# Kernel optimization log

Hardware: AMD Instinct MI355X
Metric: run time of the kernel (lower is better)

The kernel has to match this reference:

```python
import jax, jax.numpy as jnp
import numpy as np

CH = 128
MID = CH // 4  # 32
B, H, W = 16, 128, 128


def _phi(x):
    # elu(x) + 1 (alpha=1)
    return jax.nn.elu(x) + 1.0


def setup_inputs() -> dict:
    key = jax.random.key(0)
    ks = jax.random.split(key, 6)
    x = jax.random.normal(ks[0], (B, CH, H, W), dtype=jnp.float32)
    Wq = jax.random.normal(ks[1], (MID, CH), dtype=jnp.float32) * 0.05
    Wk = jax.random.normal(ks[2], (MID, CH), dtype=jnp.float32) * 0.05
    Wv = jax.random.normal(ks[3], (MID, CH), dtype=jnp.float32) * 0.05
    Wout = jax.random.normal(ks[4], (CH, MID), dtype=jnp.float32) * 0.05
    gamma = jnp.ones((CH,), dtype=jnp.float32)
    beta = jnp.zeros((CH,), dtype=jnp.float32)
    return {"x": x, "Wq": Wq, "Wk": Wk, "Wv": Wv, "Wout": Wout,
            "gamma": gamma, "beta": beta}


def reference(x, Wq, Wk, Wv, Wout, gamma, beta):
    b, c, h, w = x.shape
    n = h * w
    xf = x.reshape(b, c, n)                      # [B, C, N]
    # 1x1 convs == channel matmuls
    Q = _phi(jnp.einsum('mc,bcn->bmn', Wq, xf))  # [B, M, N]
    K = _phi(jnp.einsum('mc,bcn->bmn', Wk, xf))  # [B, M, N]
    V = jnp.einsum('mc,bcn->bmn', Wv, xf)        # [B, M, N]
    # KV-first linear attention
    KV = jnp.einsum('bmn,bvn->bmv', K, V)        # [B, M, M]
    out = jnp.einsum('bmv,bvn->bmn', KV, Q) / (n + 1e-6)  # [B, M, N]
    Ks = jnp.sum(K, axis=-1, keepdims=True)      # [B, M, 1]
    denom = jnp.sum(Q * Ks, axis=1, keepdims=True) + 1e-6  # [B, 1, N]
    out = out / denom
    # output 1x1 conv
    y = jnp.einsum('cm,bmn->bcn', Wout, out).reshape(b, c, h, w)
    # BatchNorm2d (training-mode forward: batch statistics, biased var, eps=1e-5)
    mean = jnp.mean(y, axis=(0, 2, 3), keepdims=True)
    var = jnp.var(y, axis=(0, 2, 3), keepdims=True)
    y = (y - mean) * jax.lax.rsqrt(var + 1e-5)
    y = y * gamma[None, :, None, None] + beta[None, :, None, None]
    return y
```

## Files before the change

### kernel.cpp

```cpp
#include <hip/hip_runtime.h>

#define BB 16
#define CC 128
#define MM 32
#define NN 16384

#define WS_KV     0
#define WS_KS     16384
#define WS_SQ     16896
#define WS_QQ     17408
#define WS_YSUM   33792
#define WS_YSQ    33920
#define WS_ACCEND 34048
#define WS_W2     34304

typedef __bf16 bf16x8 __attribute__((ext_vector_type(8)));
typedef __bf16 bf16x4 __attribute__((ext_vector_type(4)));
typedef float  f32x16 __attribute__((ext_vector_type(16)));

union B8 { bf16x8 v8; bf16x4 v4[2]; };

__device__ __forceinline__ float phi_f(float z) {
    return z > 0.f ? z + 1.f : __expf(z);
}

__global__ void zero_kernel(float* ws) {
    const int i = blockIdx.x * 256 + threadIdx.x;
    if (i < (WS_ACCEND / 4)) {
        float4 z; z.x = 0.f; z.y = 0.f; z.z = 0.f; z.w = 0.f;
        ((float4*)ws)[i] = z;
    }
}

__global__ __launch_bounds__(256) void projmfma_kernel(
    const float* __restrict__ x,
    const float* __restrict__ Wq, const float* __restrict__ Wk,
    const float* __restrict__ Wv,
    float* ws, float* __restrict__ qout)
{
    __shared__ __align__(16) char smem[55296];
    __bf16* Xh  = (__bf16*)smem;
    __bf16* Xl  = (__bf16*)(smem + 17408);
    __bf16* ktH = (__bf16*)(smem + 34816);
    __bf16* ktL = (__bf16*)(smem + 39936);
    __bf16* vtH = (__bf16*)(smem + 45056);
    __bf16* vtL = (__bf16*)(smem + 50176);

    const int b = blockIdx.y;
    const int t = threadIdx.x;
    const int w = t >> 6;
    const int l = t & 63;
    const int g = l >> 5;
    const int ln31 = l & 31;

    bf16x8 wh[8], wl[8];
    if (w < 3) {
        const float* Wm = (w == 0) ? Wq : (w == 1) ? Wk : Wv;
        const float* wr = Wm + ln31 * CC;
        #pragma unroll
        for (int kt = 0; kt < 8; ++kt) {
            const int k0 = 16 * kt + 8 * g;
            #pragma unroll
            for (int j = 0; j < 8; ++j) {
                const float f = wr[k0 + j];
                const __bf16 h = (__bf16)f;
                wh[kt][j] = h;
                wl[kt][j] = (__bf16)(f - (float)h);
            }
        }
    }

    f32x16 kvA, ksA;
    bf16x8 ones;
    #pragma unroll
    for (int i = 0; i < 16; ++i) { kvA[i] = 0.f; ksA[i] = 0.f; }
    #pragma unroll
    for (int j = 0; j < 8; ++j) ones[j] = (__bf16)1.0f;

    const int px = t & 31;
    const int cb = t >> 5;

    const float* xbase = x + (size_t)b * CC * NN + (blockIdx.x << 9) + px;

    float xbuf[16];
    #pragma unroll
    for (int j = 0; j < 16; ++j)
        xbuf[j] = xbase[(size_t)(cb * 16 + j) * NN];
    {
        __bf16 hbuf[16], lbuf[16];
        #pragma unroll
        for (int j = 0; j < 16; ++j) {
            const float f = xbuf[j];
            const __bf16 h = (__bf16)f;
            hbuf[j] = h;
            lbuf[j] = (__bf16)(f - (float)h);
        }
        *(bf16x8*)&Xh[px * 136 + cb * 16]     = *(bf16x8*)&hbuf[0];
        *(bf16x8*)&Xh[px * 136 + cb * 16 + 8] = *(bf16x8*)&hbuf[8];
        *(bf16x8*)&Xl[px * 136 + cb * 16]     = *(bf16x8*)&lbuf[0];
        *(bf16x8*)&Xl[px * 136 + cb * 16 + 8] = *(bf16x8*)&lbuf[8];
    }
    __syncthreads();

    for (int tile = 0; tile < 16; ++tile) {
        const int cur = tile & 1;
        const int n0 = (blockIdx.x << 9) + (tile << 5);

        if (tile < 15) {
            const float* xp = xbase + ((tile + 1) << 5);
            #pragma unroll
            for (int j = 0; j < 16; ++j)
                xbuf[j] = xp[(size_t)(cb * 16 + j) * NN];
        }

        f32x16 acc;
        if (w < 3) {
            #pragma unroll
            for (int i = 0; i < 16; ++i) acc[i] = 0.f;
            const __bf16* xh = Xh + cur * 4352 + ln31 * 136;
            const __bf16* xl = Xl + cur * 4352 + ln31 * 136;
            #pragma unroll
            for (int kt = 0; kt < 8; ++kt) {
                const int k0 = 16 * kt + 8 * g;
                const bf16x8 bh = *(const bf16x8*)&xh[k0];
                const bf16x8 bl = *(const bf16x8*)&xl[k0];
                acc = __builtin_amdgcn_mfma_f32_32x32x16_bf16(wh[kt], bh, acc, 0, 0, 0);
                acc = __builtin_amdgcn_mfma_f32_32x32x16_bf16(wh[kt], bl, acc, 0, 0, 0);
                acc = __builtin_amdgcn_mfma_f32_32x32x16_bf16(wl[kt], bh, acc, 0, 0, 0);
            }
        } else if (tile > 0) {
            const int pbuf = (cur ^ 1) * 1280;
            const __bf16* khp = ktH + pbuf + ln31 * 40;
            const __bf16* klp = ktL + pbuf + ln31 * 40;
            const __bf16* vhp = vtH + pbuf + ln31 * 40;
            const __bf16* vlp = vtL + pbuf + ln31 * 40;
            #pragma unroll
            for (int s = 0; s < 2; ++s) {
                const int k0 = s * 16 + g * 8;
                const bf16x8 akh = *(const bf16x8*)&khp[k0];
                const bf16x8 akl = *(const bf16x8*)&klp[k0];
                const bf16x8 bvh = *(const bf16x8*)&vhp[k0];
                const bf16x8 bvl = *(const bf16x8*)&vlp[k0];
                kvA = __builtin_amdgcn_mfma_f32_32x32x16_bf16(akh, bvh, kvA, 0, 0, 0);
                kvA = __builtin_amdgcn_mfma_f32_32x32x16_bf16(akh, bvl, kvA, 0, 0, 0);
                kvA = __builtin_amdgcn_mfma_f32_32x32x16_bf16(akl, bvh, kvA, 0, 0, 0);
                ksA = __builtin_amdgcn_mfma_f32_32x32x16_bf16(akh, ones, ksA, 0, 0, 0);
                ksA = __builtin_amdgcn_mfma_f32_32x32x16_bf16(akl, ones, ksA, 0, 0, 0);
            }
        }

        if (w == 0) {
            float* qp = qout + (size_t)b * CC * NN + n0 + ln31;
            #pragma unroll
            for (int i = 0; i < 16; ++i) {
                const int r = (i & 3) + 8 * (i >> 2) + 4 * g;
                qp[(size_t)r * NN] = phi_f(acc[i]);
            }
        } else if (w == 1) {
            __bf16* kh = ktH + cur * 1280;
            __bf16* kl = ktL + cur * 1280;
            #pragma unroll
            for (int i = 0; i < 16; ++i) {
                const int r = (i & 3) + 8 * (i >> 2) + 4 * g;
                const float f = phi_f(acc[i]);
                const __bf16 h = (__bf16)f;
                kh[r * 40 + ln31] = h;
                kl[r * 40 + ln31] = (__bf16)(f - (float)h);
            }
        } else if (w == 2) {
            __bf16* vh = vtH + cur * 1280;
            __bf16* vl = vtL + cur * 1280;
            #pragma unroll
            for (int i = 0; i < 16; ++i) {
                const int r = (i & 3) + 8 * (i >> 2) + 4 * g;
                const float f = acc[i];
                const __bf16 h = (__bf16)f;
                vh[r * 40 + ln31] = h;
                vl[r * 40 + ln31] = (__bf16)(f - (float)h);
            }
        }

        if (tile < 15) {
            const int nxt = cur ^ 1;
            __bf16 hbuf[16], lbuf[16];
            #pragma unroll
            for (int j = 0; j < 16; ++j) {
                const float f = xbuf[j];
                const __bf16 h = (__bf16)f;
                hbuf[j] = h;
                lbuf[j] = (__bf16)(f - (float)h);
            }
            *(bf16x8*)&Xh[nxt * 4352 + px * 136 + cb * 16]     = *(bf16x8*)&hbuf[0];
            *(bf16x8*)&Xh[nxt * 4352 + px * 136 + cb * 16 + 8] = *(bf16x8*)&hbuf[8];
            *(bf16x8*)&Xl[nxt * 4352 + px * 136 + cb * 16]     = *(bf16x8*)&lbuf[0];
            *(bf16x8*)&Xl[nxt * 4352 + px * 136 + cb * 16 + 8] = *(bf16x8*)&lbuf[8];
        }
        __syncthreads();
    }

    if (w == 3) {
        const int pbuf = 1280;
        const __bf16* khp = ktH + pbuf + ln31 * 40;
        const __bf16* klp = ktL + pbuf + ln31 * 40;
        const __bf16* vhp = vtH + pbuf + ln31 * 40;
        const __bf16* vlp = vtL + pbuf + ln31 * 40;
        #pragma unroll
        for (int s = 0; s < 2; ++s) {
            const int k0 = s * 16 + g * 8;
            const bf16x8 akh = *(const bf16x8*)&khp[k0];
            const bf16x8 akl = *(const bf16x8*)&klp[k0];
            const bf16x8 bvh = *(const bf16x8*)&vhp[k0];
            const bf16x8 bvl = *(const bf16x8*)&vlp[k0];
            kvA = __builtin_amdgcn_mfma_f32_32x32x16_bf16(akh, bvh, kvA, 0, 0, 0);
            kvA = __builtin_amdgcn_mfma_f32_32x32x16_bf16(akh, bvl, kvA, 0, 0, 0);
            kvA = __builtin_amdgcn_mfma_f32_32x32x16_bf16(akl, bvh, kvA, 0, 0, 0);
            ksA = __builtin_amdgcn_mfma_f32_32x32x16_bf16(akh, ones, ksA, 0, 0, 0);
            ksA = __builtin_amdgcn_mfma_f32_32x32x16_bf16(akl, ones, ksA, 0, 0, 0);
        }
        float* kvb = ws + WS_KV + (b << 10);
        #pragma unroll
        for (int i = 0; i < 16; ++i) {
            const int r = (i & 3) + 8 * (i >> 2) + 4 * g;
            atomicAdd(&kvb[r * 32 + ln31], kvA[i]);
        }
        if (ln31 == 0) {
            #pragma unroll
            for (int i = 0; i < 16; ++i) {
                const int r = (i & 3) + 8 * (i >> 2) + 4 * g;
                atomicAdd(&ws[WS_KS + (b << 5) + r], ksA[i]);
            }
        }
    }
}

__global__ __launch_bounds__(256) void qq_kernel(const float* qsrc, float* ws) {
    __shared__ __align__(16) char qsm[33792];
    __bf16* Qh = (__bf16*)qsm;
    __bf16* Ql = (__bf16*)(qsm + 16896);
    float*  red   = (float*)qsm;
    float*  sqred = (float*)(qsm + 17408);

    const int b = blockIdx.y;
    const int t = threadIdx.x;
    const int w = t >> 6;
    const int l = t & 63;
    const int g = l >> 5;
    const int ln31 = l & 31;

    const float* ksb = ws + WS_KS + (b << 5);
    const int n = (blockIdx.x << 8) + t;
    const float* qp = qsrc + (size_t)b * CC * NN + n;

    float qa[32];
    #pragma unroll
    for (int m = 0; m < 32; ++m) qa[m] = qp[(size_t)m * NN];

    float denom = 1e-6f;
    #pragma unroll
    for (int m = 0; m < 32; ++m) denom = fmaf(qa[m], ksb[m], denom);
    const float inv = 1.0f / (16384.0f * denom);
    #pragma unroll
    for (int m = 0; m < 32; ++m) qa[m] *= inv;

    #pragma unroll
    for (int m = 0; m < 32; ++m) {
        const __bf16 h = (__bf16)qa[m];
        Qh[m * 264 + t] = h;
        Ql[m * 264 + t] = (__bf16)(qa[m] - (float)h);
    }
    __syncthreads();

    f32x16 qqA, sqA;
    bf16x8 ones;
    #pragma unroll
    for (int i = 0; i < 16; ++i) { qqA[i] = 0.f; sqA[i] = 0.f; }
    #pragma unroll
    for (int j = 0; j < 8; ++j) ones[j] = (__bf16)1.0f;

    #pragma unroll
    for (int sub = 0; sub < 2; ++sub) {
        #pragma unroll
        for (int s = 0; s < 2; ++s) {
            const int k0 = (w << 6) + (sub << 5) + s * 16 + g * 8;
            const bf16x8 ah = *(const bf16x8*)&Qh[ln31 * 264 + k0];
            const bf16x8 al = *(const bf16x8*)&Ql[ln31 * 264 + k0];
            qqA = __builtin_amdgcn_mfma_f32_32x32x16_bf16(ah, ah, qqA, 0, 0, 0);
            qqA = __builtin_amdgcn_mfma_f32_32x32x16_bf16(ah, al, qqA, 0, 0, 0);
            qqA = __builtin_amdgcn_mfma_f32_32x32x16_bf16(al, ah, qqA, 0, 0, 0);
            sqA = __builtin_amdgcn_mfma_f32_32x32x16_bf16(ah, ones, sqA, 0, 0, 0);
            sqA = __builtin_amdgcn_mfma_f32_32x32x16_bf16(al, ones, sqA, 0, 0, 0);
        }
    }
    __syncthreads();

    #pragma unroll
    for (int i = 0; i < 16; ++i) red[t * 17 + i] = qqA[i];
    if (ln31 == 0) {
        #pragma unroll
        for (int i = 0; i < 16; ++i) {
            const int r = (i & 3) + 8 * (i >> 2) + 4 * g;
            sqred[(w << 5) + r] = sqA[i];
        }
    }
    __syncthreads();
    if (t < 64) {
        float* qqb = ws + WS_QQ + (b << 10);
        #pragma unroll
        for (int i = 0; i < 16; ++i) {
            const int r = (i & 3) + 8 * (i >> 2) + 4 * g;
            const float s = red[t*17+i] + red[(t+64)*17+i] + red[(t+128)*17+i] + red[(t+192)*17+i];
            atomicAdd(&qqb[r * 32 + ln31], s);
        }
    }
    if (t < 32) {
        const float s = sqred[t] + sqred[32 + t] + sqred[64 + t] + sqred[96 + t];
        atomicAdd(&ws[WS_SQ + (b << 5) + t], s);
    }
}

__global__ __launch_bounds__(128) void bnstat_kernel(const float* __restrict__ Wout,
                                                     float* ws) {
    const int b = blockIdx.x;
    const int c = threadIdx.x;
    const float* kvb = ws + WS_KV + (b << 10);
    const float* wo  = Wout + (c << 5);
    float w[32];
    #pragma unroll
    for (int v = 0; v < 32; ++v) w[v] = 0.f;
    for (int m = 0; m < 32; ++m) {
        const float wm = wo[m];
        #pragma unroll
        for (int v = 0; v < 32; ++v) w[v] = fmaf(wm, kvb[(m << 5) + v], w[v]);
    }
    float* w2b = ws + WS_W2 + (b << 12) + (c << 5);
    #pragma unroll
    for (int v = 0; v < 32; ++v) w2b[v] = w[v];

    const float* sq = ws + WS_SQ + (b << 5);
    const float* qq = ws + WS_QQ + (b << 10);
    float mb = 0.f;
    #pragma unroll
    for (int v = 0; v < 32; ++v) mb = fmaf(w[v], sq[v], mb);
    float qf = 0.f;
    for (int u = 0; u < 32; ++u) {
        float tacc = 0.f;
        #pragma unroll
        for (int v = 0; v < 32; ++v) tacc = fmaf(qq[(u << 5) + v], w[v], tacc);
        qf = fmaf(w[u], tacc, qf);
    }
    atomicAdd(&ws[WS_YSUM + c], mb);
    atomicAdd(&ws[WS_YSQ + c], qf);
}

__global__ __launch_bounds__(256) void out_kernel(const float* qsrc, const float* ws,
                                                  const float* __restrict__ gamma,
                                                  const float* __restrict__ beta,
                                                  float* out) {
    __shared__ __align__(16) __bf16 Qh[256 * 36];
    __shared__ __align__(16) __bf16 Ql[256 * 36];
    __shared__ float scs[CC];
    __shared__ float bis[CC];

    const int b = blockIdx.y;
    const int t = threadIdx.x;
    const int w = t >> 6;
    const int l = t & 63;
    const int g = l >> 5;
    const int ln31 = l & 31;

    if (t < CC) {
        const float invBN = 1.0f / 262144.0f;
        const float mean = ws[WS_YSUM + t] * invBN;
        const float var  = ws[WS_YSQ + t] * invBN - mean * mean;
        const float s = gamma[t] * rsqrtf(var + 1e-5f);
        scs[t] = s;
        bis[t] = fmaf(-mean, s, beta[t]);
    }

    const int n = (blockIdx.x << 8) + t;
    const float* ksb = ws + WS_KS + (b << 5);

    const float* qp = qsrc + (size_t)b * CC * NN + n;
    float qa[32];
    #pragma unroll
    for (int m = 0; m < 32; ++m) qa[m] = qp[(size_t)m * NN];

    float d0 = 1e-6f;
    #pragma unroll
    for (int m = 0; m < 32; ++m) d0 = fmaf(qa[m], ksb[m], d0);
    const float inv = 1.0f / (16384.0f * d0);
    #pragma unroll
    for (int m = 0; m < 32; ++m) qa[m] *= inv;

    {
        __bf16 qh[32], ql[32];
        #pragma unroll
        for (int m = 0; m < 32; ++m) {
            const __bf16 h = (__bf16)qa[m];
            qh[m] = h;
            ql[m] = (__bf16)(qa[m] - (float)h);
        }
        #pragma unroll
        for (int i = 0; i < 8; ++i) {
            *(bf16x4*)&Qh[t * 36 + i * 4] = *(bf16x4*)&qh[i * 4];
            *(bf16x4*)&Ql[t * 36 + i * 4] = *(bf16x4*)&ql[i * 4];
        }
    }
    __syncthreads();

    const float* w2b = ws + WS_W2 + (b << 12);
    float* ob = out + (size_t)b * CC * NN + (blockIdx.x << 8);

    #pragma unroll
    for (int cb = 0; cb < 4; ++cb) {
        bf16x8 ah[2], al[2];
        #pragma unroll
        for (int kt = 0; kt < 2; ++kt) {
            const float* wp = w2b + (cb * 32 + ln31) * 32 + kt * 16 + g * 8;
            #pragma unroll
            for (int j = 0; j < 8; ++j) {
                const float f = wp[j];
                const __bf16 h = (__bf16)f;
                ah[kt][j] = h;
                al[kt][j] = (__bf16)(f - (float)h);
            }
        }
        #pragma unroll
        for (int pg = 0; pg < 2; ++pg) {
            const int px0 = (w << 6) + (pg << 5);
            f32x16 acc;
            #pragma unroll
            for (int i = 0; i < 16; ++i) acc[i] = 0.f;
            #pragma unroll
            for (int kt = 0; kt < 2; ++kt) {
                const int k0 = kt * 16 + g * 8;
                const __bf16* qhp = &Qh[(px0 + ln31) * 36 + k0];
                const __bf16* qlp = &Ql[(px0 + ln31) * 36 + k0];
                B8 bh, bl;
                bh.v4[0] = *(const bf16x4*)&qhp[0];
                bh.v4[1] = *(const bf16x4*)&qhp[4];
                bl.v4[0] = *(const bf16x4*)&qlp[0];
                bl.v4[1] = *(const bf16x4*)&qlp[4];
                acc = __builtin_amdgcn_mfma_f32_32x32x16_bf16(ah[kt], bh.v8, acc, 0, 0, 0);
                acc = __builtin_amdgcn_mfma_f32_32x32x16_bf16(ah[kt], bl.v8, acc, 0, 0, 0);
                acc = __builtin_amdgcn_mfma_f32_32x32x16_bf16(al[kt], bh.v8, acc, 0, 0, 0);
            }
            #pragma unroll
            for (int i = 0; i < 16; ++i) {
                const int r = (i & 3) + 8 * (i >> 2) + 4 * g;
                const int c = cb * 32 + r;
                const float v = fmaf(scs[c], acc[i], bis[c]);
                __builtin_nontemporal_store(v, &ob[(size_t)c * NN + px0 + ln31]);
            }
        }
    }
}

extern "C" void kernel_launch(void* const* d_in, const int* in_sizes, int n_in,
                              void* d_out, int out_size, void* d_ws, size_t ws_size,
                              hipStream_t stream) {
    const float* x     = (const float*)d_in[0];
    const float* Wq    = (const float*)d_in[1];
    const float* Wk    = (const float*)d_in[2];
    const float* Wv    = (const float*)d_in[3];
    const float* Wout  = (const float*)d_in[4];
    const float* gamma = (const float*)d_in[5];
    const float* beta  = (const float*)d_in[6];
    float* ws  = (float*)d_ws;
    float* out = (float*)d_out;

    zero_kernel<<<34, 256, 0, stream>>>(ws);
    projmfma_kernel<<<dim3(32, 16), 256, 0, stream>>>(x, Wq, Wk, Wv, ws, out);
    qq_kernel<<<dim3(64, 16), 256, 0, stream>>>(out, ws);
    bnstat_kernel<<<16, 128, 0, stream>>>(Wout, ws);
    out_kernel<<<dim3(64, 16), 256, 0, stream>>>(out, ws, gamma, beta, out);
}
```

Baseline: 114.2 us.

## Double projection block to 512 threads processing two pixel tiles per step

The projection kernel now runs 8 waves per block: two groups of four waves each handle one of two 32-pixel sub-tiles, so each loop step covers 64 pixels in 8 steps instead of 16. The x double-buffer is replaced by a single two-half staging buffer with an extra barrier per step, and the K/V transposed buffers are quadrupled in LDS. The aim is more waves in flight per CU and fewer loop iterations to hide global-load latency. In exchange LDS use grows to about 74KB, which may cap blocks per CU, and each wave group's final KV atomics double.

```diff
diff --git a/kernel.cpp b/kernel.cpp
--- a/kernel.cpp
+++ b/kernel.cpp
@@ -32,19 +32,19 @@
     }
 }
 
-__global__ __launch_bounds__(256) void projmfma_kernel(
+__global__ __launch_bounds__(512) void projmfma_kernel(
     const float* __restrict__ x,
     const float* __restrict__ Wq, const float* __restrict__ Wk,
     const float* __restrict__ Wv,
     float* ws, float* __restrict__ qout)
 {
-    __shared__ __align__(16) char smem[55296];
+    __shared__ __align__(16) char smem[75776];
     __bf16* Xh  = (__bf16*)smem;
     __bf16* Xl  = (__bf16*)(smem + 17408);
     __bf16* ktH = (__bf16*)(smem + 34816);
-    __bf16* ktL = (__bf16*)(smem + 39936);
-    __bf16* vtH = (__bf16*)(smem + 45056);
-    __bf16* vtL = (__bf16*)(smem + 50176);
+    __bf16* ktL = (__bf16*)(smem + 45056);
+    __bf16* vtH = (__bf16*)(smem + 55296);
+    __bf16* vtL = (__bf16*)(smem + 65536);
 
     const int b = blockIdx.y;
     const int t = threadIdx.x;
@@ -52,10 +52,12 @@
     const int l = t & 63;
     const int g = l >> 5;
     const int ln31 = l & 31;
+    const int wsel = w & 3;
+    const int tb = (w >> 2) & 1;
 
     bf16x8 wh[8], wl[8];
-    if (w < 3) {
-        const float* Wm = (w == 0) ? Wq : (w == 1) ? Wk : Wv;
+    if (wsel < 3) {
+        const float* Wm = (wsel == 0) ? Wq : (wsel == 1) ? Wk : Wv;
         const float* wr = Wm + ln31 * CC;
         #pragma unroll
         for (int kt = 0; kt < 8; ++kt) {
@@ -77,48 +79,52 @@
     #pragma unroll
     for (int j = 0; j < 8; ++j) ones[j] = (__bf16)1.0f;
 
-    const int px = t & 31;
-    const int cb = t >> 5;
-
-    const float* xbase = x + (size_t)b * CC * NN + (blockIdx.x << 9) + px;
+    const int half = t >> 8;
+    const int th   = t & 255;
+    const int spx  = th & 31;
+    const int scb  = th >> 5;
+
+    const float* xbase = x + (size_t)b * CC * NN + (blockIdx.x << 9)
+                       + (half << 5) + spx;
 
     float xbuf[16];
     #pragma unroll
     for (int j = 0; j < 16; ++j)
-        xbuf[j] = xbase[(size_t)(cb * 16 + j) * NN];
-    {
-        __bf16 hbuf[16], lbuf[16];
-        #pragma unroll
-        for (int j = 0; j < 16; ++j) {
-            const float f = xbuf[j];
-            const __bf16 h = (__bf16)f;
-            hbuf[j] = h;
-            lbuf[j] = (__bf16)(f - (float)h);
-        }
-        *(bf16x8*)&Xh[px * 136 + cb * 16]     = *(bf16x8*)&hbuf[0];
-        *(bf16x8*)&Xh[px * 136 + cb * 16 + 8] = *(bf16x8*)&hbuf[8];
-        *(bf16x8*)&Xl[px * 136 + cb * 16]     = *(bf16x8*)&lbuf[0];
-        *(bf16x8*)&Xl[px * 136 + cb * 16 + 8] = *(bf16x8*)&lbuf[8];
-    }
-    __syncthreads();
-
-    for (int tile = 0; tile < 16; ++tile) {
-        const int cur = tile & 1;
-        const int n0 = (blockIdx.x << 9) + (tile << 5);
-
-        if (tile < 15) {
-            const float* xp = xbase + ((tile + 1) << 5);
+        xbuf[j] = xbase[(size_t)(scb * 16 + j) * NN];
+
+    for (int p = 0; p < 8; ++p) {
+        __syncthreads();
+
+        {
+            __bf16 hbuf[16], lbuf[16];
+            #pragma unroll
+            for (int j = 0; j < 16; ++j) {
+                const float f = xbuf[j];
+                const __bf16 h = (__bf16)f;
+                hbuf[j] = h;
+                lbuf[j] = (__bf16)(f - (float)h);
+            }
+            const int xo = half * 4352 + spx * 136 + scb * 16;
+            *(bf16x8*)&Xh[xo]     = *(bf16x8*)&hbuf[0];
+            *(bf16x8*)&Xh[xo + 8] = *(bf16x8*)&hbuf[8];
+            *(bf16x8*)&Xl[xo]     = *(bf16x8*)&lbuf[0];
+            *(bf16x8*)&Xl[xo + 8] = *(bf16x8*)&lbuf[8];
+        }
+        __syncthreads();
+
+        if (p < 7) {
+            const float* xp = xbase + ((p + 1) << 6);
             #pragma unroll
             for (int j = 0; j < 16; ++j)
-                xbuf[j] = xp[(size_t)(cb * 16 + j) * NN];
+                xbuf[j] = xp[(size_t)(scb * 16 + j) * NN];
         }
 
         f32x16 acc;
-        if (w < 3) {
+        if (wsel < 3) {
             #pragma unroll
             for (int i = 0; i < 16; ++i) acc[i] = 0.f;
-            const __bf16* xh = Xh + cur * 4352 + ln31 * 136;
-            const __bf16* xl = Xl + cur * 4352 + ln31 * 136;
+            const __bf16* xh = Xh + tb * 4352 + ln31 * 136;
+            const __bf16* xl = Xl + tb * 4352 + ln31 * 136;
             #pragma unroll
             for (int kt = 0; kt < 8; ++kt) {
                 const int k0 = 16 * kt + 8 * g;
@@ -128,12 +134,12 @@
                 acc = __builtin_amdgcn_mfma_f32_32x32x16_bf16(wh[kt], bl, acc, 0, 0, 0);
                 acc = __builtin_amdgcn_mfma_f32_32x32x16_bf16(wl[kt], bh, acc, 0, 0, 0);
             }
-        } else if (tile > 0) {
-            const int pbuf = (cur ^ 1) * 1280;
-            const __bf16* khp = ktH + pbuf + ln31 * 40;
-            const __bf16* klp = ktL + pbuf + ln31 * 40;
-            const __bf16* vhp = vtH + pbuf + ln31 * 40;
-            const __bf16* vlp = vtL + pbuf + ln31 * 40;
+        } else if (p > 0) {
+            const int po = (((p & 1) ^ 1) * 2 + tb) * 1280;
+            const __bf16* khp = ktH + po + ln31 * 40;
+            const __bf16* klp = ktL + po + ln31 * 40;
+            const __bf16* vhp = vtH + po + ln31 * 40;
+            const __bf16* vlp = vtL + po + ln31 * 40;
             #pragma unroll
             for (int s = 0; s < 2; ++s) {
                 const int k0 = s * 16 + g * 8;
@@ -149,16 +155,18 @@
             }
         }
 
-        if (w == 0) {
-            float* qp = qout + (size_t)b * CC * NN + n0 + ln31;
+        const int nbase = (blockIdx.x << 9) + (p << 6) + (tb << 5);
+        if (wsel == 0) {
+            float* qp = qout + (size_t)b * CC * NN + nbase + ln31;
             #pragma unroll
             for (int i = 0; i < 16; ++i) {
                 const int r = (i & 3) + 8 * (i >> 2) + 4 * g;
                 qp[(size_t)r * NN] = phi_f(acc[i]);
             }
-        } else if (w == 1) {
-            __bf16* kh = ktH + cur * 1280;
-            __bf16* kl = ktL + cur * 1280;
+        } else if (wsel == 1) {
+            const int po = ((p & 1) * 2 + tb) * 1280;
+            __bf16* kh = ktH + po;
+            __bf16* kl = ktL + po;
             #pragma unroll
             for (int i = 0; i < 16; ++i) {
                 const int r = (i & 3) + 8 * (i >> 2) + 4 * g;
@@ -167,9 +175,10 @@
                 kh[r * 40 + ln31] = h;
                 kl[r * 40 + ln31] = (__bf16)(f - (float)h);
             }
-        } else if (w == 2) {
-            __bf16* vh = vtH + cur * 1280;
-            __bf16* vl = vtL + cur * 1280;
+        } else if (wsel == 2) {
+            const int po = ((p & 1) * 2 + tb) * 1280;
+            __bf16* vh = vtH + po;
+            __bf16* vl = vtL + po;
             #pragma unroll
             for (int i = 0; i < 16; ++i) {
                 const int r = (i & 3) + 8 * (i >> 2) + 4 * g;
@@ -179,31 +188,16 @@
                 vl[r * 40 + ln31] = (__bf16)(f - (float)h);
             }
         }
-
-        if (tile < 15) {
-            const int nxt = cur ^ 1;
-            __bf16 hbuf[16], lbuf[16];
-            #pragma unroll
-            for (int j = 0; j < 16; ++j) {
-                const float f = xbuf[j];
-                const __bf16 h = (__bf16)f;
-                hbuf[j] = h;
-                lbuf[j] = (__bf16)(f - (float)h);
-            }
-            *(bf16x8*)&Xh[nxt * 4352 + px * 136 + cb * 16]     = *(bf16x8*)&hbuf[0];
-            *(bf16x8*)&Xh[nxt * 4352 + px * 136 + cb * 16 + 8] = *(bf16x8*)&hbuf[8];
-            *(bf16x8*)&Xl[nxt * 4352 + px * 136 + cb * 16]     = *(bf16x8*)&lbuf[0];
-            *(bf16x8*)&Xl[nxt * 4352 + px * 136 + cb * 16 + 8] = *(bf16x8*)&lbuf[8];
-        }
-        __syncthreads();
-    }
-
-    if (w == 3) {
-        const int pbuf = 1280;
-        const __bf16* khp = ktH + pbuf + ln31 * 40;
-        const __bf16* klp = ktL + pbuf + ln31 * 40;
-        const __bf16* vhp = vtH + pbuf + ln31 * 40;
-        const __bf16* vlp = vtL + pbuf + ln31 * 40;
+    }
+
+    __syncthreads();
+
+    if (wsel == 3) {
+        const int po = (1 * 2 + tb) * 1280;
+        const __bf16* khp = ktH + po + ln31 * 40;
+        const __bf16* klp = ktL + po + ln31 * 40;
+        const __bf16* vhp = vtH + po + ln31 * 40;
+        const __bf16* vlp = vtL + po + ln31 * 40;
         #pragma unroll
         for (int s = 0; s < 2; ++s) {
             const int k0 = s * 16 + g * 8;
@@ -470,7 +464,7 @@
     float* out = (float*)d_out;
 
     zero_kernel<<<34, 256, 0, stream>>>(ws);
-    projmfma_kernel<<<dim3(32, 16), 256, 0, stream>>>(x, Wq, Wk, Wv, ws, out);
+    projmfma_kernel<<<dim3(32, 16), 512, 0, stream>>>(x, Wq, Wk, Wv, ws, out);
     qq_kernel<<<dim3(64, 16), 256, 0, stream>>>(out, ws);
     bnstat_kernel<<<16, 128, 0, stream>>>(Wout, ws);
     out_kernel<<<dim3(64, 16), 256, 0, stream>>>(out, ws, gamma, beta, out);
```

New measurement: 135.1 us. +18.3%, slower.
